# Kernel tuning notes

Hardware: AMD Instinct MI355X
Metric: run time of the kernel (lower is better)

Reference implementation:

```python
import jax, jax.numpy as jnp
import numpy as np

NUM_CLASSES = 81
THRESHOLD = 0.5
NEGPOS_RATIO = 3
OBJ_SCORE = 0.01
VAR0, VAR1 = 0.1, 0.2


def point_form(boxes):
    # center form (cx,cy,w,h) -> corner form (x1,y1,x2,y2)
    return jnp.concatenate([boxes[:, :2] - boxes[:, 2:] / 2,
                            boxes[:, :2] + boxes[:, 2:] / 2], axis=1)


def jaccard(a, b):
    # a: [A,4] corners, b: [B,4] corners -> IoU [A,B]
    lt = jnp.maximum(a[:, None, :2], b[None, :, :2])
    rb = jnp.minimum(a[:, None, 2:], b[None, :, 2:])
    wh = jnp.clip(rb - lt, 0.0)
    inter = wh[..., 0] * wh[..., 1]
    area_a = ((a[:, 2] - a[:, 0]) * (a[:, 3] - a[:, 1]))[:, None]
    area_b = ((b[:, 2] - b[:, 0]) * (b[:, 3] - b[:, 1]))[None, :]
    return inter / (area_a + area_b - inter)


def encode(matched, priors):
    # matched: [P,4] corner-form GT, priors: [P,4] center-form
    g_cxcy = ((matched[:, :2] + matched[:, 2:]) / 2 - priors[:, :2]) / (VAR0 * priors[:, 2:])
    g_wh = jnp.log((matched[:, 2:] - matched[:, :2]) / priors[:, 2:]) / VAR1
    return jnp.concatenate([g_cxcy, g_wh], axis=1)


def match_one(truths, labels, priors):
    # truths: [O,4] corners, labels: [O] int, priors: [P,4] center-form
    overlaps = jaccard(truths, point_form(priors))      # [O,P]
    best_prior_idx = jnp.argmax(overlaps, axis=1)       # [O]
    best_truth_overlap = jnp.max(overlaps, axis=0)      # [P]
    best_truth_idx = jnp.argmax(overlaps, axis=0)       # [P]
    # ensure every gt matches its best prior
    best_truth_overlap = best_truth_overlap.at[best_prior_idx].set(2.0)
    best_truth_idx = best_truth_idx.at[best_prior_idx].set(jnp.arange(truths.shape[0]))
    matches = truths[best_truth_idx]                    # [P,4]
    conf = jnp.where(best_truth_overlap < THRESHOLD, 0, labels[best_truth_idx].astype(jnp.int32))
    return encode(matches, priors), conf


def smooth_l1(x):
    ax = jnp.abs(x)
    return jnp.where(ax < 1.0, 0.5 * ax * ax, ax - 0.5)


def ce_per_row(logits, tgt):
    # sum-reduction cross-entropy components: logsumexp - logit[target]
    lse = jax.nn.logsumexp(logits, axis=-1)
    picked = jnp.take_along_axis(logits, tgt[..., None].astype(jnp.int32), axis=-1)[..., 0]
    return lse - picked


def setup_inputs() -> dict:
    key = jax.random.key(0)
    ks = jax.random.split(key, 8)
    B, P, O, C = 32, 24564, 16, NUM_CLASSES
    loc_data = jax.random.normal(ks[0], (B, P, 4), jnp.float32)
    conf_data = jax.random.normal(ks[1], (B, P, C), jnp.float32)
    obj_data = jax.random.normal(ks[2], (B, P, 2), jnp.float32)
    # priors in center form
    pc = jax.random.uniform(ks[3], (P, 2), jnp.float32, 0.0, 1.0)
    pwh = jax.random.uniform(ks[4], (P, 2), jnp.float32, 0.05, 0.5)
    priors = jnp.concatenate([pc, pwh], axis=1)
    # gt boxes in corner form, valid (x1<x2, y1<y2)
    tc = jax.random.uniform(ks[5], (B, O, 2), jnp.float32, 0.2, 0.8)
    twh = jax.random.uniform(ks[6], (B, O, 2), jnp.float32, 0.05, 0.3)
    truths = jnp.concatenate([jnp.clip(tc - twh / 2, 0.0, 1.0),
                              jnp.clip(tc + twh / 2, 0.0, 1.0)], axis=-1)
    labels = jax.random.randint(ks[7], (B, O), 1, C).astype(jnp.int64)
    return {"loc_data": loc_data, "conf_data": conf_data, "obj_data": obj_data,
            "priors": priors, "truths": truths, "labels": labels}


def reference(loc_data, conf_data, obj_data, priors, truths, labels):
    num, num_priors = loc_data.shape[:2]
    loc_t, conf_t = jax.vmap(match_one, in_axes=(0, 0, None))(truths, labels, priors)
    loc_t = jax.lax.stop_gradient(loc_t)      # Variable(requires_grad=False)
    conf_t = jax.lax.stop_gradient(conf_t)
    obj_t = (conf_t > 0).astype(jnp.int32)

    obj_conf = jax.lax.stop_gradient(obj_data[:, :, 1])   # .detach()
    pos = conf_t > 0
    # faithful to original (buggy) filter: (pos + neg_positive) > 2 is never true
    neg_positive = (pos.astype(jnp.int32) + (obj_conf < OBJ_SCORE).astype(jnp.int32)) > 2
    pos = pos & ~neg_positive
    pos = jnp.where(pos.sum() == 0, conf_t > 0, pos)

    # localization loss (smooth L1, sum over positives)
    l1 = smooth_l1(loc_data - loc_t).sum(-1)               # [B,P]
    loss_l = jnp.sum(jnp.where(pos, l1, 0.0))

    # objectness loss with hard negative mining
    ce_obj = ce_per_row(obj_data, obj_t)                   # [B,P]
    pos_obj = obj_t > 0
    mining_obj = jnp.where(pos_obj, 0.0, jax.lax.stop_gradient(ce_obj))
    rank_obj = jnp.argsort(jnp.argsort(-mining_obj, axis=1), axis=1)
    num_obj_pos = pos_obj.sum(1, keepdims=True)
    num_obj_neg = jnp.minimum(NEGPOS_RATIO * num_obj_pos, num_priors - 1)
    neg_obj = rank_obj < num_obj_neg
    loss_obj = jnp.sum(jnp.where(pos_obj | neg_obj, ce_obj, 0.0))

    # class confidence loss with hard negative mining
    ce_c = ce_per_row(conf_data, conf_t)                   # [B,P]
    mining_c = jnp.where(pos, 0.0, jax.lax.stop_gradient(ce_c))
    rank_c = jnp.argsort(jnp.argsort(-mining_c, axis=1), axis=1)
    num_pos = pos.sum(1, keepdims=True)
    num_neg = jnp.minimum(NEGPOS_RATIO * num_pos, num_priors - 1)
    neg = rank_c < num_neg
    loss_c = jnp.sum(jnp.where(pos | neg, ce_c, 0.0))

    N = jnp.maximum(num_pos.sum(), 1).astype(loc_data.dtype)
    N1 = jnp.maximum(num_obj_neg.sum(), 1).astype(loc_data.dtype)
    return (loss_l / N, loss_c / N, 0.4 * loss_obj / N1)
```

## Files before the change

kernel.cpp:

```cpp
#include <hip/hip_runtime.h>
#include <hip/hip_bf16.h>
#include <math.h>

#define BB 32
#define PP 24564
#define OO 16
#define CC 81
#define BP (BB * PP)
#define CHUNK 1024

typedef unsigned long long ull;

__device__ __forceinline__ float sl1(float x) {
    float ax = fabsf(x);
    return ax < 1.0f ? 0.5f * ax * ax : ax - 0.5f;
}

__device__ __forceinline__ float4 ld4u(const float* p) {
    float4 v;
    __builtin_memcpy(&v, p, 16);
    return v;
}

__device__ __forceinline__ float ald(const float* p) {
    return __hip_atomic_load(p, __ATOMIC_RELAXED, __HIP_MEMORY_SCOPE_AGENT);
}
__device__ __forceinline__ int aldi(const int* p) {
    return __hip_atomic_load(p, __ATOMIC_RELAXED, __HIP_MEMORY_SCOPE_AGENT);
}

__global__ __launch_bounds__(256) void k_match_a(
        const float* __restrict__ priors, const float* __restrict__ truths,
        ull* __restrict__ best_prior ) {
    const int b = blockIdx.y;
    const int p0 = blockIdx.x * CHUNK;
    const int tid = threadIdx.x;
    __shared__ float tr[OO][4];
    __shared__ float tarea[OO];
    __shared__ ull red[4][OO];
    if (tid < OO * 4) ((float*)tr)[tid] = truths[b * OO * 4 + tid];
    __syncthreads();
    if (tid < OO) tarea[tid] = (tr[tid][2] - tr[tid][0]) * (tr[tid][3] - tr[tid][1]);
    __syncthreads();

    float bpv[OO];
    int bpi[OO];
#pragma unroll
    for (int o = 0; o < OO; o++) { bpv[o] = -1.0f; bpi[o] = -1; }

    const int pend = (p0 + CHUNK < PP) ? p0 + CHUNK : PP;
    for (int p = p0 + tid; p < pend; p += 256) {
        const float4 pr = ((const float4*)priors)[p];
        const float x1 = pr.x - pr.z * 0.5f, y1 = pr.y - pr.w * 0.5f;
        const float x2 = pr.x + pr.z * 0.5f, y2 = pr.y + pr.w * 0.5f;
        const float parea = (x2 - x1) * (y2 - y1);
#pragma unroll
        for (int o = 0; o < OO; o++) {
            const float lx = fmaxf(tr[o][0], x1), ly = fmaxf(tr[o][1], y1);
            const float rx = fminf(tr[o][2], x2), ry = fminf(tr[o][3], y2);
            const float iw = fmaxf(rx - lx, 0.0f), ih = fmaxf(ry - ly, 0.0f);
            const float inter = iw * ih;
            const float iou = inter / (tarea[o] + parea - inter);
            if (iou > bpv[o]) { bpv[o] = iou; bpi[o] = p; }
        }
    }

    const int wave = tid >> 6;
    const int lane = tid & 63;
#pragma unroll
    for (int o = 0; o < OO; o++) {
        ull key = (bpi[o] >= 0)
            ? (((ull)__float_as_uint(bpv[o]) << 32) |
               (ull)(0xFFFFFFFFu - (unsigned)bpi[o]))
            : 0ull;
#pragma unroll
        for (int d = 32; d; d >>= 1) {
            const ull other = __shfl_xor(key, d);
            key = (other > key) ? other : key;
        }
        if (lane == 0) red[wave][o] = key;
    }
    __syncthreads();
    if (tid < OO) {
        const ull k0 = red[0][tid], k1 = red[1][tid];
        const ull k2 = red[2][tid], k3 = red[3][tid];
        ull m = k0 > k1 ? k0 : k1;
        const ull m2 = k2 > k3 ? k2 : k3;
        m = m > m2 ? m : m2;
        if (m != 0ull) atomicMax(&best_prior[b * OO + tid], m);
    }
}

__global__ __launch_bounds__(256) void k_ce2(
        const float* __restrict__ conf, const float* __restrict__ obj,
        const float* __restrict__ loc, const float* __restrict__ priors,
        const float* __restrict__ truths, const int* __restrict__ labels,
        const ull* __restrict__ best_prior,
        float* __restrict__ mining ,
        int* __restrict__ num_posS ,
        float* __restrict__ accS  ) {
    const int tid = threadIdx.x;
    const int tile = blockIdx.x;
    const int row0 = tile * 64;
    const int r = tid >> 2;
    const int part = tid & 3;
    const int row = row0 + r;
    const float* rowp = conf + (size_t)row * CC;
    const int c0 = part * 20;

    const float4 v0 = ld4u(rowp + c0);
    const float4 v1 = ld4u(rowp + c0 + 4);
    const float4 v2 = ld4u(rowp + c0 + 8);
    const float4 v3 = ld4u(rowp + c0 + 12);
    const float4 v4 = ld4u(rowp + c0 + 16);
    const float ex = (part == 3) ? rowp[80] : 0.0f;

    float m = v0.x;
    m = fmaxf(m, v0.y); m = fmaxf(m, v0.z); m = fmaxf(m, v0.w);
    m = fmaxf(m, v1.x); m = fmaxf(m, v1.y); m = fmaxf(m, v1.z); m = fmaxf(m, v1.w);
    m = fmaxf(m, v2.x); m = fmaxf(m, v2.y); m = fmaxf(m, v2.z); m = fmaxf(m, v2.w);
    m = fmaxf(m, v3.x); m = fmaxf(m, v3.y); m = fmaxf(m, v3.z); m = fmaxf(m, v3.w);
    m = fmaxf(m, v4.x); m = fmaxf(m, v4.y); m = fmaxf(m, v4.z); m = fmaxf(m, v4.w);
    if (part == 3) m = fmaxf(m, ex);
    m = fmaxf(m, __shfl_xor(m, 1));
    m = fmaxf(m, __shfl_xor(m, 2));

    float s = 0.0f;
    s += __expf(v0.x - m); s += __expf(v0.y - m); s += __expf(v0.z - m); s += __expf(v0.w - m);
    s += __expf(v1.x - m); s += __expf(v1.y - m); s += __expf(v1.z - m); s += __expf(v1.w - m);
    s += __expf(v2.x - m); s += __expf(v2.y - m); s += __expf(v2.z - m); s += __expf(v2.w - m);
    s += __expf(v3.x - m); s += __expf(v3.y - m); s += __expf(v3.z - m); s += __expf(v3.w - m);
    s += __expf(v4.x - m); s += __expf(v4.y - m); s += __expf(v4.z - m); s += __expf(v4.w - m);
    if (part == 3) s += __expf(ex - m);
    s += __shfl_xor(s, 1);
    s += __shfl_xor(s, 2);
    const float lse = m + __logf(s);

    const int b = row / PP;
    bool pos = false;
    float my_l = 0.0f, my_co = 0.0f, my_cc = 0.0f;
    if (part == 0) {
        const int p = row - b * PP;
        const float4 pr = ((const float4*)priors)[p];
        const float x1 = pr.x - pr.z * 0.5f, y1 = pr.y - pr.w * 0.5f;
        const float x2 = pr.x + pr.z * 0.5f, y2 = pr.y + pr.w * 0.5f;
        const float parea = (x2 - x1) * (y2 - y1);
        float best = -1.0f;
        int ti = 0;
        const float4* trb = (const float4*)truths + b * OO;
#pragma unroll
        for (int o = 0; o < OO; o++) {
            const float4 t = trb[o];
            const float ta = (t.z - t.x) * (t.w - t.y);
            const float lx = fmaxf(t.x, x1), ly = fmaxf(t.y, y1);
            const float rx = fminf(t.z, x2), ry = fminf(t.w, y2);
            const float iw = fmaxf(rx - lx, 0.0f), ih = fmaxf(ry - ly, 0.0f);
            const float inter = iw * ih;
            const float iou = inter / (ta + parea - inter);
            if (iou > best) { best = iou; ti = o; }
        }
        float ov = best;
#pragma unroll
        for (int o = 0; o < OO; o++) {
            const unsigned fp = 0xFFFFFFFFu -
                (unsigned)(best_prior[b * OO + o] & 0xFFFFFFFFull);
            if (fp == (unsigned)p) { ti = o; ov = 2.0f; }
        }

        const int lbl = labels[b * OO + ti];
        const int tgt = (ov < 0.5f) ? 0 : lbl;
        const float ce_c = lse - rowp[tgt];

        const float2 o2 = ((const float2*)obj)[row];
        const float mo = fmaxf(o2.x, o2.y);
        const float lse_o = mo + __logf(__expf(o2.x - mo) + __expf(o2.y - mo));
        pos = tgt > 0;
        const float ce_o = lse_o - (pos ? o2.y : o2.x);

        mining[BP + row] = pos ? 0.0f : ce_c;
        mining[row]      = pos ? 0.0f : ce_o;

        if (pos) {
            my_co = ce_o;
            my_cc = ce_c;
            const float4 t = trb[ti];
            const float gcx = ((t.x + t.z) * 0.5f - pr.x) / (0.1f * pr.z);
            const float gcy = ((t.y + t.w) * 0.5f - pr.y) / (0.1f * pr.w);
            const float gw = logf((t.z - t.x) / pr.z) / 0.2f;
            const float gh = logf((t.w - t.y) / pr.w) / 0.2f;
            const float4 ld = ((const float4*)loc)[row];
            my_l = sl1(ld.x - gcx) + sl1(ld.y - gcy) +
                   sl1(ld.z - gw) + sl1(ld.w - gh);
        }
    }

    const int lane = tid & 63;
    const int w = tid >> 6;
    const ull mpos = __ballot(pos);
    const int bw0 = __shfl(b, 0);
    const ull mb1 = __ballot(b != bw0);
#pragma unroll
    for (int d = 32; d; d >>= 1) {
        my_l  += __shfl_down(my_l,  d);
        my_co += __shfl_down(my_co, d);
        my_cc += __shfl_down(my_cc, d);
    }
    if (lane == 0 && mpos) {
        const int stripe = tile * 4 + w;
        const int cnt0 = __popcll(mpos & ~mb1);
        const int cnt1 = __popcll(mpos &  mb1);
        int* nps = num_posS + (stripe & 7) * BB;
        if (cnt0) atomicAdd(&nps[bw0], cnt0);
        if (cnt1) atomicAdd(&nps[bw0 + 1], cnt1);
        float* slot = accS + (size_t)(stripe & 63) * 32;
        atomicAdd(slot + 0, my_l);
        atomicAdd(slot + 1, my_co);
        atomicAdd(slot + 2, my_cc);
    }
}

__global__ __launch_bounds__(1024) void k_select_final(
        const float* __restrict__ mining ,
        const int* __restrict__ num_posS ,
        float* __restrict__ acc ,
        int* __restrict__ done_ctr,
        const float* __restrict__ accS ,
        float* __restrict__ out) {
    const int arr = blockIdx.x >> 5;
    const int b = blockIdx.x & 31;
    const int tid = threadIdx.x;
    const int wv = tid >> 6;
    int np = 0;
#pragma unroll
    for (int s = 0; s < 8; s++) np += num_posS[s * BB + b];
    long long k64 = 3LL * np;
    const int k = (int)(k64 < (long long)(PP - 1) ? k64 : (long long)(PP - 1));

    __shared__ unsigned histw[16][256];
    __shared__ unsigned hist[256];
    __shared__ unsigned s_prefix;
    __shared__ int s_krem;
    __shared__ float wsum[16];
    __shared__ unsigned wcnt[16];
    __shared__ int s_last;

    if (k > 0) {
        const float* x = mining + ((size_t)arr * BB + b) * PP;
        if (tid == 0) { s_prefix = 0u; s_krem = k; }

        for (int shift = 24; shift >= 0; shift -= 8) {
            __syncthreads();
            for (int i = tid; i < 16 * 256; i += 1024) ((unsigned*)histw)[i] = 0u;
            const unsigned prefix = s_prefix;
            const unsigned pmask = (shift == 24) ? 0u : (0xFFFFFFFFu << (shift + 8));
            __syncthreads();
            for (int i = tid; i < PP; i += 1024) {
                const unsigned u = __float_as_uint(x[i]);
                if ((u & pmask) == prefix)
                    atomicAdd(&histw[wv][(u >> shift) & 255u], 1u);
            }
            __syncthreads();
            if (tid < 256) {
                unsigned s = 0;
#pragma unroll
                for (int w = 0; w < 16; w++) s += histw[w][tid];
                hist[tid] = s;
            }
            __syncthreads();
            if (tid == 0) {
                const int krem = s_krem;
                unsigned cum = 0;
                int sel = 0;
                for (int byte = 255; byte >= 0; byte--) {
                    const unsigned h = hist[byte];
                    if (cum + h >= (unsigned)krem) { sel = byte; break; }
                    cum += h;
                }
                s_krem = krem - (int)cum;
                s_prefix = prefix | ((unsigned)sel << shift);
            }
        }
        __syncthreads();

        const unsigned t = s_prefix;
        float lsum = 0.0f;
        unsigned lcnt = 0;
        for (int i = tid; i < PP; i += 1024) {
            const float v = x[i];
            if (__float_as_uint(v) > t) { lsum += v; lcnt++; }
        }
#pragma unroll
        for (int d = 32; d; d >>= 1) {
            lsum += __shfl_down(lsum, d);
            lcnt += __shfl_down(lcnt, d);
        }
        if ((tid & 63) == 0) { wsum[wv] = lsum; wcnt[wv] = lcnt; }
        __syncthreads();
        if (tid == 0) {
            float ts = 0.0f;
            unsigned tc = 0;
#pragma unroll
            for (int w = 0; w < 16; w++) { ts += wsum[w]; tc += wcnt[w]; }
            const float tsum = ts + (float)(k - (int)tc) * __uint_as_float(t);
            atomicAdd(&acc[3 + arr], tsum);
        }
    }

    __syncthreads();
    __threadfence();
    if (tid == 0) s_last = (atomicAdd(done_ctr, 1) == 63);
    __syncthreads();
    if (s_last) {
        __threadfence();
        if (tid < 64) {
            float sl = ald(&accS[tid * 32 + 0]);
            float so = ald(&accS[tid * 32 + 1]);
            float sc = ald(&accS[tid * 32 + 2]);
            int np_b = 0, k_b = 0;
            if (tid < BB) {
#pragma unroll
                for (int s2 = 0; s2 < 8; s2++) np_b += aldi(&num_posS[s2 * BB + tid]);
                long long kk = 3LL * np_b;
                k_b = (int)(kk < (long long)(PP - 1) ? kk : (long long)(PP - 1));
            }
#pragma unroll
            for (int d = 32; d; d >>= 1) {
                sl += __shfl_down(sl, d);
                so += __shfl_down(so, d);
                sc += __shfl_down(sc, d);
                np_b += __shfl_down(np_b, d);
                k_b  += __shfl_down(k_b,  d);
            }
            if (tid == 0) {
                const float fN = (float)(np_b > 1 ? np_b : 1);
                const float fN1 = (float)(k_b > 1 ? k_b : 1);
                const float a3 = ald(&acc[3]);
                const float a4 = ald(&acc[4]);
                out[0] = sl / fN;
                out[1] = (sc + a4) / fN;
                out[2] = 0.4f * (so + a3) / fN1;
            }
        }
    }
}

extern "C" void kernel_launch(void* const* d_in, const int* in_sizes, int n_in,
                              void* d_out, int out_size, void* d_ws, size_t ws_size,
                              hipStream_t stream) {
    const float* loc_data  = (const float*)d_in[0];
    const float* conf_data = (const float*)d_in[1];
    const float* obj_data  = (const float*)d_in[2];
    const float* priors    = (const float*)d_in[3];
    const float* truths    = (const float*)d_in[4];
    const int*   labels    = (const int*)d_in[5];
    float* out = (float*)d_out;

    float* ws_f = (float*)d_ws;
    float* mining = ws_f;
    const size_t S = 2 * (size_t)BP;
    ull*   best_prior = (ull*)(ws_f + S);
    int*   num_posS   = (int*)(ws_f + S + 1024);
    float* acc        = ws_f + S + 1280;
    int*   done_ctr   = (int*)(ws_f + S + 1288);
    float* accS       = ws_f + S + 2048;

    hipMemsetAsync((void*)best_prior, 0, 16384, stream);

    dim3 mg((PP + CHUNK - 1) / CHUNK, BB);
    k_match_a<<<mg, 256, 0, stream>>>(priors, truths, best_prior);

    k_ce2<<<BP / 64, 256, 0, stream>>>(conf_data, obj_data, loc_data, priors,
                                       truths, labels, best_prior,
                                       mining, num_posS, accS);

    k_select_final<<<64, 1024, 0, stream>>>(mining, num_posS, acc, done_ctr,
                                            accS, out);
}
```

Before: 467.7 us.

## Cache mining rows in registers for radix select and drop memset

The select kernel now loads each row of mining values into 24 registers per thread once and reuses them across all four radix histogram passes and the final sum, instead of re-reading global memory on every pass. The match kernel runs one block per batch over all priors and writes best_prior directly, with no atomics. Block 0 zeroes the counter and accumulator workspace, which replaces the separate hipMemsetAsync. The cost is much less parallelism in matching (32 blocks) and higher register pressure in the select kernel.

```diff
diff --git a/kernel.cpp b/kernel.cpp
--- a/kernel.cpp
+++ b/kernel.cpp
@@ -7,7 +7,6 @@
 #define OO 16
 #define CC 81
 #define BP (BB * PP)
-#define CHUNK 1024
 
 typedef unsigned long long ull;
 
@@ -29,15 +28,20 @@
     return __hip_atomic_load(p, __ATOMIC_RELAXED, __HIP_MEMORY_SCOPE_AGENT);
 }
 
-__global__ __launch_bounds__(256) void k_match_a(
+__global__ __launch_bounds__(256) void k_match(
         const float* __restrict__ priors, const float* __restrict__ truths,
-        ull* __restrict__ best_prior ) {
-    const int b = blockIdx.y;
-    const int p0 = blockIdx.x * CHUNK;
+        ull* __restrict__ best_prior ,
+        float* __restrict__ zero_base ) {
+    const int b = blockIdx.x;
     const int tid = threadIdx.x;
     __shared__ float tr[OO][4];
     __shared__ float tarea[OO];
     __shared__ ull red[4][OO];
+
+    if (b == 0) {
+        for (int i = tid; i < 3072; i += 256) zero_base[i] = 0.0f;
+    }
+
     if (tid < OO * 4) ((float*)tr)[tid] = truths[b * OO * 4 + tid];
     __syncthreads();
     if (tid < OO) tarea[tid] = (tr[tid][2] - tr[tid][0]) * (tr[tid][3] - tr[tid][1]);
@@ -48,8 +52,7 @@
 #pragma unroll
     for (int o = 0; o < OO; o++) { bpv[o] = -1.0f; bpi[o] = -1; }
 
-    const int pend = (p0 + CHUNK < PP) ? p0 + CHUNK : PP;
-    for (int p = p0 + tid; p < pend; p += 256) {
+    for (int p = tid; p < PP; p += 256) {
         const float4 pr = ((const float4*)priors)[p];
         const float x1 = pr.x - pr.z * 0.5f, y1 = pr.y - pr.w * 0.5f;
         const float x2 = pr.x + pr.z * 0.5f, y2 = pr.y + pr.w * 0.5f;
@@ -87,7 +90,7 @@
         ull m = k0 > k1 ? k0 : k1;
         const ull m2 = k2 > k3 ? k2 : k3;
         m = m > m2 ? m : m2;
-        if (m != 0ull) atomicMax(&best_prior[b * OO + tid], m);
+        best_prior[b * OO + tid] = m;
     }
 }
 
@@ -219,7 +222,7 @@
     }
 }
 
-__global__ __launch_bounds__(1024) void k_select_final(
+__global__ __launch_bounds__(1024, 1) void k_select_final(
         const float* __restrict__ mining ,
         const int* __restrict__ num_posS ,
         float* __restrict__ acc ,
@@ -246,6 +249,12 @@
 
     if (k > 0) {
         const float* x = mining + ((size_t)arr * BB + b) * PP;
+        float rg[24];
+#pragma unroll
+        for (int j = 0; j < 23; j++) rg[j] = x[j * 1024 + tid];
+        const bool v23 = tid < (PP - 23 * 1024);
+        rg[23] = v23 ? x[23 * 1024 + tid] : 0.0f;
+
         if (tid == 0) { s_prefix = 0u; s_krem = k; }
 
         for (int shift = 24; shift >= 0; shift -= 8) {
@@ -254,10 +263,13 @@
             const unsigned prefix = s_prefix;
             const unsigned pmask = (shift == 24) ? 0u : (0xFFFFFFFFu << (shift + 8));
             __syncthreads();
-            for (int i = tid; i < PP; i += 1024) {
-                const unsigned u = __float_as_uint(x[i]);
-                if ((u & pmask) == prefix)
-                    atomicAdd(&histw[wv][(u >> shift) & 255u], 1u);
+#pragma unroll
+            for (int j = 0; j < 24; j++) {
+                if (j < 23 || v23) {
+                    const unsigned u = __float_as_uint(rg[j]);
+                    if ((u & pmask) == prefix)
+                        atomicAdd(&histw[wv][(u >> shift) & 255u], 1u);
+                }
             }
             __syncthreads();
             if (tid < 256) {
@@ -285,9 +297,11 @@
         const unsigned t = s_prefix;
         float lsum = 0.0f;
         unsigned lcnt = 0;
-        for (int i = tid; i < PP; i += 1024) {
-            const float v = x[i];
-            if (__float_as_uint(v) > t) { lsum += v; lcnt++; }
+#pragma unroll
+        for (int j = 0; j < 24; j++) {
+            if (j < 23 || v23) {
+                if (__float_as_uint(rg[j]) > t) { lsum += rg[j]; lcnt++; }
+            }
         }
 #pragma unroll
         for (int d = 32; d; d >>= 1) {
@@ -363,11 +377,9 @@
     float* acc        = ws_f + S + 1280;
     int*   done_ctr   = (int*)(ws_f + S + 1288);
     float* accS       = ws_f + S + 2048;
-
-    hipMemsetAsync((void*)best_prior, 0, 16384, stream);
-
-    dim3 mg((PP + CHUNK - 1) / CHUNK, BB);
-    k_match_a<<<mg, 256, 0, stream>>>(priors, truths, best_prior);
+    float* zero_base  = ws_f + S + 1024;
+
+    k_match<<<BB, 256, 0, stream>>>(priors, truths, best_prior, zero_base);
 
     k_ce2<<<BP / 64, 256, 0, stream>>>(conf_data, obj_data, loc_data, priors,
                                        truths, labels, best_prior,
```

Measured after the change: 565.8 us. 1.21x slower.
